# Performance work log

Measured on AMD Instinct MI355X. Metric: run time of the kernel, lower is better.

The kernel has to match this reference:

```python
import jax, jax.numpy as jnp
import numpy as np

HID = 64
PRE = 14


def _lstm_last(x, Wih, Whh, b):
    # x: (B, T, F) batch_first; single-layer torch LSTM; returns last hidden (B, H)
    H = Whh.shape[1]
    def step(carry, xt):
        h, c = carry
        g = xt @ Wih.T + h @ Whh.T + b  # gates order i,f,g,o (torch convention)
        i, f, gg, o = jnp.split(g, 4, axis=-1)
        c = jax.nn.sigmoid(f) * c + jax.nn.sigmoid(i) * jnp.tanh(gg)
        h = jax.nn.sigmoid(o) * jnp.tanh(c)
        return (h, c), None
    h0 = jnp.zeros((x.shape[0], H), x.dtype)
    (h, _), _ = jax.lax.scan(step, (h0, h0), jnp.swapaxes(x, 0, 1))
    return h


def _sircell(beta, gamma, c, sir):
    # beta,gamma: (B,N,1); c: (B,N,N); sir: (B,N,3); beta_incorporated=False branch
    eps = 1e-8
    S, I, R = sir[..., 0:1], sir[..., 1:2], sir[..., 2:3]
    Ntot = jnp.maximum(S + I + R, eps)
    infection = c @ I                      # (B,N,1) graph diffusion of infected
    dS = -beta * S / Ntot * infection
    dI = -dS - gamma * I
    dR = gamma * I
    S_t = jnp.maximum(S + dS, 0.0)
    I_t = jnp.maximum(I + dI, 0.0)
    R_t = jnp.maximum(R + dR, 0.0)
    scale = Ntot / jnp.maximum(S_t + I_t + R_t, eps)
    I_new = jnp.maximum(-dS, 0.0)
    return jnp.concatenate([I_new, S_t * scale, I_t * scale, R_t * scale], axis=-1)


def reference(x_s, x, bWih, bWhh, bb, bfW, bfb, gWih, gWhh, gb, gfW, gfb, cWih, cWhh, cb, cfW, cfb):
    B, T, N, F = x_s.shape
    P = bfW.shape[0]
    xs = jnp.transpose(x_s, (0, 2, 1, 3)).reshape(B * N, T, F)
    betas = jax.nn.sigmoid(_lstm_last(xs, bWih, bWhh, bb) @ bfW.T + bfb).reshape(B, N, P, 1)
    gammas = jax.nn.sigmoid(_lstm_last(xs, gWih, gWhh, gb) @ gfW.T + gfb).reshape(B, N, P, 1)
    xst = jnp.transpose(x_s, (0, 2, 1, 3))                       # (B,N,T,F)
    Hi = jnp.broadcast_to(xst[:, :, None], (B, N, N, T, F))
    Hj = jnp.broadcast_to(xst[:, None], (B, N, N, T, F))
    edge = jnp.concatenate([Hi, Hj], -1).reshape(B * N * N, T, 2 * F)
    cij = jax.nn.sigmoid(_lstm_last(edge, cWih, cWhh, cb) @ cfW.T + cfb).reshape(B, N, N, P)
    cij = jax.nn.softmax(jnp.transpose(cij, (0, 3, 1, 2)), axis=-1)  # (B,P,N,N)
    cs = jnp.transpose(cij, (0, 2, 1, 3))                            # (B,N,P,N)

    def step(sir, inp):
        bt, gt, ct = inp
        nsir = _sircell(bt, gt, ct, sir)
        return nsir[:, :, 1:], nsir

    _, outs = jax.lax.scan(
        step, x[:, -1],
        (jnp.transpose(betas, (2, 0, 1, 3)),
         jnp.transpose(gammas, (2, 0, 1, 3)),
         jnp.transpose(cs, (2, 0, 1, 3))))
    out = jnp.transpose(outs, (1, 0, 2, 3))                          # (B,P,N,4)
    epi = jnp.transpose(jnp.concatenate([betas, gammas, cs], -1), (0, 2, 1, 3))  # (B,P,N,N+2)
    return out[..., 2:3], epi, out[..., 1:], out[..., 0:1]


def setup_inputs() -> dict:
    key = jax.random.key(0)
    ks = jax.random.split(key, 20)
    B, T, N, F = 4, 12, 128, 3
    H, P = HID, PRE
    s = 1.0 / np.sqrt(H)
    def u(k, shape):
        return jax.random.uniform(k, shape, jnp.float32, -s, s)
    inp = {
        'x_s': jax.random.normal(ks[0], (B, T, N, F), jnp.float32),
        'x': jax.random.uniform(ks[1], (B, T, N, F), jnp.float32),
        'bWih': u(ks[2], (4 * H, F)), 'bWhh': u(ks[3], (4 * H, H)), 'bb': u(ks[4], (4 * H,)),
        'bfW': u(ks[5], (P, H)), 'bfb': u(ks[6], (P,)),
        'gWih': u(ks[7], (4 * H, F)), 'gWhh': u(ks[8], (4 * H, H)), 'gb': u(ks[9], (4 * H,)),
        'gfW': u(ks[10], (P, H)), 'gfb': u(ks[11], (P,)),
        'cWih': u(ks[12], (4 * H, 2 * F)), 'cWhh': u(ks[13], (4 * H, H)), 'cb': u(ks[14], (4 * H,)),
        'cfW': u(ks[15], (P, H)), 'cfb': u(ks[16], (P,)),
    }
    return inp
```

## Files before the change

kernel.cpp:

```cpp
#include <hip/hip_runtime.h>

#define TT 12
#define NN 128
#define BB 4
#define PP 14

typedef __attribute__((ext_vector_type(8))) short short8;
typedef __attribute__((ext_vector_type(4))) float f32x4;
typedef __attribute__((ext_vector_type(2))) float float2v;
typedef __attribute__((ext_vector_type(2))) unsigned uint2v;

__device__ inline unsigned short f2bf(float x){
  unsigned u = __builtin_bit_cast(unsigned, x);
  u += 0x7fffu + ((u >> 16) & 1u);
  return (unsigned short)(u >> 16);
}
__device__ inline float bf2f(unsigned short h){
  unsigned u = ((unsigned)h) << 16;
  return __builtin_bit_cast(float, u);
}
__device__ inline float fexp2(float x){ return __builtin_amdgcn_exp2f(x); }
__device__ inline float frcp(float x){ return __builtin_amdgcn_rcpf(x); }
__device__ inline float sigf(float x){ return frcp(1.0f + fexp2(x * -1.44269504f)); }

__device__ inline float2v exp2v(float2v x){
  float2v r; r[0]=__builtin_amdgcn_exp2f(x[0]); r[1]=__builtin_amdgcn_exp2f(x[1]); return r;
}
__device__ inline float2v rcpv1(float2v x){
  float r = frcp(x[0]*x[1]);
  float2v o; o[0] = x[1]*r; o[1] = x[0]*r; return o;
}

__global__ __launch_bounds__(512) void lstm_all(
    const float* __restrict__ x_s,
    const float* __restrict__ bWih, const float* __restrict__ bWhh, const float* __restrict__ bb_,
    const float* __restrict__ bfW,  const float* __restrict__ bfb,
    const float* __restrict__ gWih, const float* __restrict__ gWhh, const float* __restrict__ gb_,
    const float* __restrict__ gfW,  const float* __restrict__ gfb,
    const float* __restrict__ cWih, const float* __restrict__ cWhh, const float* __restrict__ cb_,
    const float* __restrict__ cfW,  const float* __restrict__ cfb,
    float* __restrict__ out_epi)
{
  __shared__ __align__(16) unsigned short wfrag[48*64*8];
  __shared__ __align__(16) char hbuf[2*8192];
  __shared__ __align__(16) unsigned short xext[TT*64*8];
  __shared__ unsigned short fw_lds[PP*64];
  __shared__ float fb_lds[PP];

  const int tid = threadIdx.x;
  const int l = tid & 63;
  const int wv = tid >> 6;
  const int w_h = wv & 3;
  const int half = wv >> 2;
  const int col = l & 15, q = l >> 4;

  const int rot = (col & 7) << 4;
  const int rowA = half*32 + col,  rowB = half*32 + 16 + col;
  const int r0offA = rowA*128 + (((q<<4) + rot) & 127);
  const int r1offA = rowA*128 + ((64 + (q<<4) + rot) & 127);
  const int r0offB = rowB*128 + (((q<<4) + rot) & 127);
  const int r1offB = rowB*128 + ((64 + (q<<4) + rot) & 127);
  const int wroffA = rowA*128 + ((w_h*32 + q*8 + rot) & 127);
  const int wroffB = rowB*128 + ((w_h*32 + q*8 + rot) & 127);

  int g = blockIdx.x;
  int mode; const float *Wih, *Whh, *bias, *fW, *fb;
  if (g < 1024)      { mode=0; Wih=cWih; Whh=cWhh; bias=cb_; fW=cfW; fb=cfb; }
  else if (g < 1032) { mode=1; g-=1024; Wih=bWih; Whh=bWhh; bias=bb_; fW=bfW; fb=bfb; }
  else               { mode=2; g-=1032; Wih=gWih; Whh=gWhh; bias=gb_; fW=gfW; fb=gfb; }

  int b, i=0, s0;
  if (mode==0) { b = g >> 8; int rem = g & 255; i = rem >> 1; s0 = (rem & 1) << 6; }
  else         { b = g >> 1; s0 = (g & 1) << 6; }

  for (int task = tid; task < TT*64; task += 512) {
    int t = task >> 6, m = task & 63;
    unsigned short* dst = &xext[(t*64+m)*8];
    float v0=0,v1=0,v2=0,v3=0,v4=0,v5=0,v6=0,v7=0;
    if (mode==0) {
      const float* xi = x_s + ((b*TT + t)*NN + i)*3;
      const float* xj = x_s + ((b*TT + t)*NN + (s0+m))*3;
      v0=xi[0]; v1=xi[1]; v2=xi[2]; v3=xj[0]; v4=xj[1]; v5=xj[2]; v6=1.f;
    } else {
      const float* xn = x_s + ((b*TT + t)*NN + (s0+m))*3;
      v0=xn[0]; v1=xn[1]; v2=xn[2]; v3=1.f;
    }
    dst[0]=f2bf(v0); dst[1]=f2bf(v1); dst[2]=f2bf(v2); dst[3]=f2bf(v3);
    dst[4]=f2bf(v4); dst[5]=f2bf(v5); dst[6]=f2bf(v6); dst[7]=f2bf(v7);
  }
  for (int idx = tid; idx < 2048; idx += 512) ((unsigned*)hbuf)[idx] = 0;
  for (int idx = tid; idx < PP*64; idx += 512) fw_lds[idx] = f2bf(fW[idx]);
  if (tid < PP) fb_lds[tid] = fb[tid];

  for (int slot = tid; slot < 48*64; slot += 512) {
    int tile = slot >> 6, lane = slot & 63;
    int w_hs = tile / 12, rem = tile % 12, gt = rem / 3, kt = rem % 3;
    float sc = (gt==2) ? 2.88539008f : -1.44269504f;
    int gate = gt*64 + w_hs*16 + (lane & 15);
    int qq = lane >> 4;
    short8 fr = {0,0,0,0,0,0,0,0};
    if (kt < 2) {
      const float* src = Whh + gate*64 + kt*32 + qq*8;
      #pragma unroll
      for (int jj = 0; jj < 8; ++jj) fr[jj] = (short)f2bf(src[jj]*sc);
    } else if (qq == 0) {
      if (mode==0) {
        fr[0]=(short)f2bf(Wih[gate*6+0]*sc); fr[1]=(short)f2bf(Wih[gate*6+1]*sc); fr[2]=(short)f2bf(Wih[gate*6+2]*sc);
        fr[3]=(short)f2bf(Wih[gate*6+3]*sc); fr[4]=(short)f2bf(Wih[gate*6+4]*sc); fr[5]=(short)f2bf(Wih[gate*6+5]*sc);
        fr[6]=(short)f2bf(bias[gate]*sc);
      } else {
        fr[0]=(short)f2bf(Wih[gate*3+0]*sc); fr[1]=(short)f2bf(Wih[gate*3+1]*sc); fr[2]=(short)f2bf(Wih[gate*3+2]*sc);
        fr[3]=(short)f2bf(bias[gate]*sc);
      }
    }
    *(short8*)&wfrag[slot*8] = fr;
  }

  __syncthreads();

  float2v cA0 = {0.f,0.f}, cA1 = {0.f,0.f}, cB0 = {0.f,0.f}, cB1 = {0.f,0.f};

#define MM(acc, aop, bop) acc = __builtin_amdgcn_mfma_f32_16x16x32_bf16(aop, bop, acc, 0,0,0)
#define CELL(cvar, hvar, fF, fI, fG, fO) { \
    float2v Ei = exp2v(fI), Ef = exp2v(fF), Eg = exp2v(fG), Eo = exp2v(fO); \
    float2v t1 = (Ei + 1.0f) * (Eg + 1.0f); \
    float2v pf = Ef + 1.0f; \
    float2v num = cvar * t1 + pf * (Eg - 1.0f); \
    cvar = num * rcpv1(pf * t1); \
    float2v Ec = exp2v(cvar * 2.88539008f); \
    hvar = (Ec - 1.0f) * rcpv1((Ec + 1.0f) * (Eo + 1.0f)); }
#define GATETILE(gt, accA, accB) { \
    short8 f0 = *(const short8*)&wfrag[((w_h*12 + (gt)*3 + 0)*64 + l)*8]; \
    short8 f1 = *(const short8*)&wfrag[((w_h*12 + (gt)*3 + 1)*64 + l)*8]; \
    short8 fx = *(const short8*)&wfrag[((w_h*12 + (gt)*3 + 2)*64 + l)*8]; \
    MM(accA, f0, b0a); MM(accB, f0, b0b); \
    MM(accA, f1, b1a); MM(accB, f1, b1b); \
    MM(accA, fx, bxa); MM(accB, fx, bxb); }

  for (int t = 0; t < TT; ++t) {
    const char* rb = hbuf + ((t & 1) ? 8192 : 0);
    char* wbp      = hbuf + ((t & 1) ? 0 : 8192);
    short8 b0a = *(const short8*)(rb + r0offA);
    short8 b1a = *(const short8*)(rb + r1offA);
    short8 b0b = *(const short8*)(rb + r0offB);
    short8 b1b = *(const short8*)(rb + r1offB);
    short8 bxa = *(const short8*)&xext[(t*64 + half*32 + col)*8];
    short8 bxb = *(const short8*)&xext[(t*64 + half*32 + 16 + col)*8];
    f32x4 Fa = {0.f,0.f,0.f,0.f}, Ia = Fa, Ga = Fa, Oa = Fa;
    f32x4 Fb = Fa, Ib = Fa, Gb = Fa, Ob = Fa;
    GATETILE(1, Fa, Fb);
    GATETILE(0, Ia, Ib);
    GATETILE(2, Ga, Gb);
    GATETILE(3, Oa, Ob);

    {
      float2v f0 = {Fa[0],Fa[1]}, f1 = {Fa[2],Fa[3]};
      float2v i0 = {Ia[0],Ia[1]}, i1 = {Ia[2],Ia[3]};
      float2v g0v = {Ga[0],Ga[1]}, g1v = {Ga[2],Ga[3]};
      float2v o0 = {Oa[0],Oa[1]}, o1 = {Oa[2],Oa[3]};
      float2v h0, h1;
      CELL(cA0, h0, f0, i0, g0v, o0);
      CELL(cA1, h1, f1, i1, g1v, o1);
      unsigned plo, phi;
      asm("v_cvt_pk_bf16_f32 %0, %1, %2" : "=v"(plo) : "v"(h0[0]), "v"(h0[1]));
      asm("v_cvt_pk_bf16_f32 %0, %1, %2" : "=v"(phi) : "v"(h1[0]), "v"(h1[1]));
      uint2v pv = {plo, phi};
      *(uint2v*)(wbp + wroffA) = pv;
    }
    {
      float2v f0 = {Fb[0],Fb[1]}, f1 = {Fb[2],Fb[3]};
      float2v i0 = {Ib[0],Ib[1]}, i1 = {Ib[2],Ib[3]};
      float2v g0v = {Gb[0],Gb[1]}, g1v = {Gb[2],Gb[3]};
      float2v o0 = {Ob[0],Ob[1]}, o1 = {Ob[2],Ob[3]};
      float2v h0, h1;
      CELL(cB0, h0, f0, i0, g0v, o0);
      CELL(cB1, h1, f1, i1, g1v, o1);
      unsigned plo, phi;
      asm("v_cvt_pk_bf16_f32 %0, %1, %2" : "=v"(plo) : "v"(h0[0]), "v"(h0[1]));
      asm("v_cvt_pk_bf16_f32 %0, %1, %2" : "=v"(phi) : "v"(h1[0]), "v"(h1[1]));
      uint2v pv = {plo, phi};
      *(uint2v*)(wbp + wroffB) = pv;
    }
    __syncthreads();
  }
#undef MM
#undef CELL
#undef GATETILE

  const char* hfin = hbuf;
  for (int task = tid; task < 64*PP; task += 512) {
    int seq = task & 63, p = task >> 6;
    int rot2 = (seq & 7) << 4;
    float dot = fb_lds[p];
    #pragma unroll
    for (int kc = 0; kc < 8; ++kc) {
      short8 v = *(const short8*)(hfin + seq*128 + (((kc<<4) + rot2) & 127));
      #pragma unroll
      for (int jj = 0; jj < 8; ++jj)
        dot += bf2f((unsigned short)v[jj]) * bf2f(fw_lds[p*64 + kc*8 + jj]);
    }
    float val = sigf(dot);
    if (mode==0) {
      out_epi[(size_t)((b*PP + p)*NN + i)*130 + 2 + (s0+seq)] = val;
    } else if (mode==1) {
      out_epi[(size_t)((b*PP + p)*NN + (s0+seq))*130 + 0] = val;
    } else {
      out_epi[(size_t)((b*PP + p)*NN + (s0+seq))*130 + 1] = val;
    }
  }
}

__global__ __launch_bounds__(256) void softmax_epi(float* __restrict__ out_epi)
{
  int row = blockIdx.x*4 + (threadIdx.x >> 6);
  int l = threadIdx.x & 63;
  float* epi = out_epi + (size_t)row*130;
  float v0 = epi[2+l], v1 = epi[2+64+l];
  float e0 = fexp2(v0*1.44269504f), e1 = fexp2(v1*1.44269504f);
  float s = e0 + e1;
  #pragma unroll
  for (int off = 32; off; off >>= 1) s += __shfl_xor(s, off);
  float inv = frcp(s);
  epi[2+l] = e0*inv; epi[2+64+l] = e1*inv;
}

__global__ __launch_bounds__(1024) void sir_scan(
    const float* __restrict__ x,
    const float* __restrict__ epi,
    float* __restrict__ out0, float* __restrict__ out2, float* __restrict__ out3)
{
  __shared__ float Ish[NN];
  int b = blockIdx.x;
  int tid = threadIdx.x;
  int i = tid >> 3, q = tid & 7;
  const float* x0 = x + ((b*TT + 11)*NN + i)*3;
  float S = x0[0], I = x0[1], R = x0[2];
  if (q == 0) Ish[i] = I;

  float2v v[8], vn[8];
  {
    const float* crow = epi + (size_t)((b*PP + 0)*NN + i)*130 + 2 + q*16;
    #pragma unroll
    for (int jj = 0; jj < 8; ++jj) v[jj] = *(const float2v*)(crow + jj*2);
  }
  __syncthreads();
  for (int p = 0; p < PP; ++p) {
    if (p+1 < PP) {
      const float* crow = epi + (size_t)((b*PP + p+1)*NN + i)*130 + 2 + q*16;
      #pragma unroll
      for (int jj = 0; jj < 8; ++jj) vn[jj] = *(const float2v*)(crow + jj*2);
    }
    float part = 0.f;
    #pragma unroll
    for (int jj = 0; jj < 8; ++jj)
      part += v[jj][0]*Ish[q*16 + jj*2] + v[jj][1]*Ish[q*16 + jj*2 + 1];
    part += __shfl_xor(part, 1);
    part += __shfl_xor(part, 2);
    part += __shfl_xor(part, 4);
    __syncthreads();
    if (q == 0) {
      const float* erow = epi + (size_t)((b*PP + p)*NN + i)*130;
      float beta  = erow[0];
      float gamma = erow[1];
      float Ntot = fmaxf(S+I+R, 1e-8f);
      float dS = -beta*S/Ntot*part;
      float dI = -dS - gamma*I;
      float dR = gamma*I;
      float St = fmaxf(S+dS, 0.f), It = fmaxf(I+dI, 0.f), Rt = fmaxf(R+dR, 0.f);
      float scale = Ntot / fmaxf(St+It+Rt, 1e-8f);
      float Inew = fmaxf(-dS, 0.f);
      int o = (b*PP+p)*NN + i;
      float Sn = St*scale, In = It*scale, Rn = Rt*scale;
      out0[o] = In;
      out2[o*3+0] = Sn; out2[o*3+1] = In; out2[o*3+2] = Rn;
      out3[o] = Inew;
      S = Sn; I = In; R = Rn;
      Ish[i] = I;
    }
    #pragma unroll
    for (int jj = 0; jj < 8; ++jj) v[jj] = vn[jj];
    __syncthreads();
  }
}

extern "C" void kernel_launch(void* const* d_in, const int* in_sizes, int n_in,
                              void* d_out, int out_size, void* d_ws, size_t ws_size,
                              hipStream_t stream) {
  const float* x_s  = (const float*)d_in[0];
  const float* x    = (const float*)d_in[1];
  const float* bWih = (const float*)d_in[2];
  const float* bWhh = (const float*)d_in[3];
  const float* bb_  = (const float*)d_in[4];
  const float* bfW  = (const float*)d_in[5];
  const float* bfb  = (const float*)d_in[6];
  const float* gWih = (const float*)d_in[7];
  const float* gWhh = (const float*)d_in[8];
  const float* gb_  = (const float*)d_in[9];
  const float* gfW  = (const float*)d_in[10];
  const float* gfb  = (const float*)d_in[11];
  const float* cWih = (const float*)d_in[12];
  const float* cWhh = (const float*)d_in[13];
  const float* cb_  = (const float*)d_in[14];
  const float* cfW  = (const float*)d_in[15];
  const float* cfb  = (const float*)d_in[16];

  float* out  = (float*)d_out;
  float* out0 = out;
  float* epi  = out + 7168;
  float* out2 = out + 7168 + 931840;
  float* out3 = out + 7168 + 931840 + 21504;

  hipLaunchKernelGGL(lstm_all, dim3(1040), dim3(512), 0, stream,
      x_s, bWih,bWhh,bb_,bfW,bfb, gWih,gWhh,gb_,gfW,gfb, cWih,cWhh,cb_,cfW,cfb,
      epi);
  hipLaunchKernelGGL(softmax_epi, dim3(1792), dim3(256), 0, stream, epi);
  hipLaunchKernelGGL(sir_scan, dim3(4), dim3(1024), 0, stream,
      x, epi, out0, out2, out3);
}
```

Before: 107.4 us.

## Give each wave its own sequences so LSTM steps skip block barriers

The LSTM kernel now runs 256 threads per block instead of 512. Each wave owns 16 sequences and computes all four hidden-slice gate tiles for them, keeping its hidden state in a private LDS scratch area. This removes the double-buffered shared hidden state and the __syncthreads at every time step, and the final projection is done per wave. In exchange each wave issues twice as many serial MFMAs per step. Block-level parallelism per CU also drops, because the large LDS weight footprint still limits how many blocks fit per CU.

```diff
diff --git a/kernel.cpp b/kernel.cpp
--- a/kernel.cpp
+++ b/kernel.cpp
@@ -31,7 +31,7 @@
   float2v o; o[0] = x[1]*r; o[1] = x[0]*r; return o;
 }
 
-__global__ __launch_bounds__(512) void lstm_all(
+__global__ __launch_bounds__(256) void lstm_all(
     const float* __restrict__ x_s,
     const float* __restrict__ bWih, const float* __restrict__ bWhh, const float* __restrict__ bb_,
     const float* __restrict__ bfW,  const float* __restrict__ bfb,
@@ -42,7 +42,7 @@
     float* __restrict__ out_epi)
 {
   __shared__ __align__(16) unsigned short wfrag[48*64*8];
-  __shared__ __align__(16) char hbuf[2*8192];
+  __shared__ __align__(16) char hscratch[4*2048];
   __shared__ __align__(16) unsigned short xext[TT*64*8];
   __shared__ unsigned short fw_lds[PP*64];
   __shared__ float fb_lds[PP];
@@ -50,18 +50,12 @@
   const int tid = threadIdx.x;
   const int l = tid & 63;
   const int wv = tid >> 6;
-  const int w_h = wv & 3;
-  const int half = wv >> 2;
   const int col = l & 15, q = l >> 4;
 
   const int rot = (col & 7) << 4;
-  const int rowA = half*32 + col,  rowB = half*32 + 16 + col;
-  const int r0offA = rowA*128 + (((q<<4) + rot) & 127);
-  const int r1offA = rowA*128 + ((64 + (q<<4) + rot) & 127);
-  const int r0offB = rowB*128 + (((q<<4) + rot) & 127);
-  const int r1offB = rowB*128 + ((64 + (q<<4) + rot) & 127);
-  const int wroffA = rowA*128 + ((w_h*32 + q*8 + rot) & 127);
-  const int wroffB = rowB*128 + ((w_h*32 + q*8 + rot) & 127);
+  char* hs = hscratch + wv*2048;
+  const int r0off = col*128 + (((q<<4) + rot) & 127);
+  const int r1off = col*128 + ((64 + (q<<4) + rot) & 127);
 
   int g = blockIdx.x;
   int mode; const float *Wih, *Whh, *bias, *fW, *fb;
@@ -73,7 +67,7 @@
   if (mode==0) { b = g >> 8; int rem = g & 255; i = rem >> 1; s0 = (rem & 1) << 6; }
   else         { b = g >> 1; s0 = (g & 1) << 6; }
 
-  for (int task = tid; task < TT*64; task += 512) {
+  for (int task = tid; task < TT*64; task += 256) {
     int t = task >> 6, m = task & 63;
     unsigned short* dst = &xext[(t*64+m)*8];
     float v0=0,v1=0,v2=0,v3=0,v4=0,v5=0,v6=0,v7=0;
@@ -88,11 +82,11 @@
     dst[0]=f2bf(v0); dst[1]=f2bf(v1); dst[2]=f2bf(v2); dst[3]=f2bf(v3);
     dst[4]=f2bf(v4); dst[5]=f2bf(v5); dst[6]=f2bf(v6); dst[7]=f2bf(v7);
   }
-  for (int idx = tid; idx < 2048; idx += 512) ((unsigned*)hbuf)[idx] = 0;
-  for (int idx = tid; idx < PP*64; idx += 512) fw_lds[idx] = f2bf(fW[idx]);
+  for (int idx = tid; idx < PP*64; idx += 256) fw_lds[idx] = f2bf(fW[idx]);
   if (tid < PP) fb_lds[tid] = fb[tid];
-
-  for (int slot = tid; slot < 48*64; slot += 512) {
+  for (int idx = l; idx < 512; idx += 64) ((unsigned*)hs)[idx] = 0;
+
+  for (int slot = tid; slot < 48*64; slot += 256) {
     int tile = slot >> 6, lane = slot & 63;
     int w_hs = tile / 12, rem = tile % 12, gt = rem / 3, kt = rem % 3;
     float sc = (gt==2) ? 2.88539008f : -1.44269504f;
@@ -118,7 +112,9 @@
 
   __syncthreads();
 
-  float2v cA0 = {0.f,0.f}, cA1 = {0.f,0.f}, cB0 = {0.f,0.f}, cB1 = {0.f,0.f};
+  float2v c0s[4], c1s[4];
+  #pragma unroll
+  for (int s = 0; s < 4; ++s) { c0s[s] = (float2v){0.f,0.f}; c1s[s] = (float2v){0.f,0.f}; }
 
 #define MM(acc, aop, bop) acc = __builtin_amdgcn_mfma_f32_16x16x32_bf16(aop, bop, acc, 0,0,0)
 #define CELL(cvar, hvar, fF, fI, fG, fO) { \
@@ -129,77 +125,57 @@
     cvar = num * rcpv1(pf * t1); \
     float2v Ec = exp2v(cvar * 2.88539008f); \
     hvar = (Ec - 1.0f) * rcpv1((Ec + 1.0f) * (Eo + 1.0f)); }
-#define GATETILE(gt, accA, accB) { \
-    short8 f0 = *(const short8*)&wfrag[((w_h*12 + (gt)*3 + 0)*64 + l)*8]; \
-    short8 f1 = *(const short8*)&wfrag[((w_h*12 + (gt)*3 + 1)*64 + l)*8]; \
-    short8 fx = *(const short8*)&wfrag[((w_h*12 + (gt)*3 + 2)*64 + l)*8]; \
-    MM(accA, f0, b0a); MM(accB, f0, b0b); \
-    MM(accA, f1, b1a); MM(accB, f1, b1b); \
-    MM(accA, fx, bxa); MM(accB, fx, bxb); }
 
   for (int t = 0; t < TT; ++t) {
-    const char* rb = hbuf + ((t & 1) ? 8192 : 0);
-    char* wbp      = hbuf + ((t & 1) ? 0 : 8192);
-    short8 b0a = *(const short8*)(rb + r0offA);
-    short8 b1a = *(const short8*)(rb + r1offA);
-    short8 b0b = *(const short8*)(rb + r0offB);
-    short8 b1b = *(const short8*)(rb + r1offB);
-    short8 bxa = *(const short8*)&xext[(t*64 + half*32 + col)*8];
-    short8 bxb = *(const short8*)&xext[(t*64 + half*32 + 16 + col)*8];
-    f32x4 Fa = {0.f,0.f,0.f,0.f}, Ia = Fa, Ga = Fa, Oa = Fa;
-    f32x4 Fb = Fa, Ib = Fa, Gb = Fa, Ob = Fa;
-    GATETILE(1, Fa, Fb);
-    GATETILE(0, Ia, Ib);
-    GATETILE(2, Ga, Gb);
-    GATETILE(3, Oa, Ob);
-
-    {
-      float2v f0 = {Fa[0],Fa[1]}, f1 = {Fa[2],Fa[3]};
-      float2v i0 = {Ia[0],Ia[1]}, i1 = {Ia[2],Ia[3]};
-      float2v g0v = {Ga[0],Ga[1]}, g1v = {Ga[2],Ga[3]};
-      float2v o0 = {Oa[0],Oa[1]}, o1 = {Oa[2],Oa[3]};
+    short8 b0 = *(const short8*)(hs + r0off);
+    short8 b1 = *(const short8*)(hs + r1off);
+    short8 bx = *(const short8*)&xext[(t*64 + wv*16 + col)*8];
+    #pragma unroll
+    for (int s = 0; s < 4; ++s) {
+      const unsigned short* wb = &wfrag[((s*12)*64 + l)*8];
+      f32x4 Fv = {0.f,0.f,0.f,0.f}, Iv = Fv, Gv = Fv, Ov = Fv;
+      MM(Fv, *(const short8*)(wb + 3*512), b0);
+      MM(Iv, *(const short8*)(wb + 0*512), b0);
+      MM(Gv, *(const short8*)(wb + 6*512), b0);
+      MM(Ov, *(const short8*)(wb + 9*512), b0);
+      MM(Fv, *(const short8*)(wb + 4*512), b1);
+      MM(Iv, *(const short8*)(wb + 1*512), b1);
+      MM(Gv, *(const short8*)(wb + 7*512), b1);
+      MM(Ov, *(const short8*)(wb + 10*512), b1);
+      MM(Fv, *(const short8*)(wb + 5*512), bx);
+      MM(Iv, *(const short8*)(wb + 2*512), bx);
+      MM(Gv, *(const short8*)(wb + 8*512), bx);
+      MM(Ov, *(const short8*)(wb + 11*512), bx);
+      float2v f0 = {Fv[0],Fv[1]}, f1 = {Fv[2],Fv[3]};
+      float2v i0 = {Iv[0],Iv[1]}, i1 = {Iv[2],Iv[3]};
+      float2v g0v = {Gv[0],Gv[1]}, g1v = {Gv[2],Gv[3]};
+      float2v o0 = {Ov[0],Ov[1]}, o1 = {Ov[2],Ov[3]};
       float2v h0, h1;
-      CELL(cA0, h0, f0, i0, g0v, o0);
-      CELL(cA1, h1, f1, i1, g1v, o1);
+      CELL(c0s[s], h0, f0, i0, g0v, o0);
+      CELL(c1s[s], h1, f1, i1, g1v, o1);
       unsigned plo, phi;
       asm("v_cvt_pk_bf16_f32 %0, %1, %2" : "=v"(plo) : "v"(h0[0]), "v"(h0[1]));
       asm("v_cvt_pk_bf16_f32 %0, %1, %2" : "=v"(phi) : "v"(h1[0]), "v"(h1[1]));
       uint2v pv = {plo, phi};
-      *(uint2v*)(wbp + wroffA) = pv;
-    }
-    {
-      float2v f0 = {Fb[0],Fb[1]}, f1 = {Fb[2],Fb[3]};
-      float2v i0 = {Ib[0],Ib[1]}, i1 = {Ib[2],Ib[3]};
-      float2v g0v = {Gb[0],Gb[1]}, g1v = {Gb[2],Gb[3]};
-      float2v o0 = {Ob[0],Ob[1]}, o1 = {Ob[2],Ob[3]};
-      float2v h0, h1;
-      CELL(cB0, h0, f0, i0, g0v, o0);
-      CELL(cB1, h1, f1, i1, g1v, o1);
-      unsigned plo, phi;
-      asm("v_cvt_pk_bf16_f32 %0, %1, %2" : "=v"(plo) : "v"(h0[0]), "v"(h0[1]));
-      asm("v_cvt_pk_bf16_f32 %0, %1, %2" : "=v"(phi) : "v"(h1[0]), "v"(h1[1]));
-      uint2v pv = {plo, phi};
-      *(uint2v*)(wbp + wroffB) = pv;
-    }
-    __syncthreads();
+      *(uint2v*)(hs + col*128 + ((s*32 + q*8 + rot) & 127)) = pv;
+    }
   }
 #undef MM
 #undef CELL
-#undef GATETILE
-
-  const char* hfin = hbuf;
-  for (int task = tid; task < 64*PP; task += 512) {
-    int seq = task & 63, p = task >> 6;
-    int rot2 = (seq & 7) << 4;
+
+  for (int task = l; task < 16*PP; task += 64) {
+    int sl = task & 15, p = task >> 4;
+    int rot2 = (sl & 7) << 4;
     float dot = fb_lds[p];
     #pragma unroll
     for (int kc = 0; kc < 8; ++kc) {
-      short8 v = *(const short8*)(hfin + seq*128 + (((kc<<4) + rot2) & 127));
+      short8 v = *(const short8*)(hs + sl*128 + (((kc<<4) + rot2) & 127));
       #pragma unroll
       for (int jj = 0; jj < 8; ++jj)
         dot += bf2f((unsigned short)v[jj]) * bf2f(fw_lds[p*64 + kc*8 + jj]);
     }
     float val = sigf(dot);
+    int seq = wv*16 + sl;
     if (mode==0) {
       out_epi[(size_t)((b*PP + p)*NN + i)*130 + 2 + (s0+seq)] = val;
     } else if (mode==1) {
@@ -310,7 +286,7 @@
   float* out2 = out + 7168 + 931840;
   float* out3 = out + 7168 + 931840 + 21504;
 
-  hipLaunchKernelGGL(lstm_all, dim3(1040), dim3(512), 0, stream,
+  hipLaunchKernelGGL(lstm_all, dim3(1040), dim3(256), 0, stream,
       x_s, bWih,bWhh,bb_,bfW,bfb, gWih,gWhh,gb_,gfW,gfb, cWih,cWhh,cb_,cfW,cfb,
       epi);
   hipLaunchKernelGGL(softmax_epi, dim3(1792), dim3(256), 0, stream, epi);
```

After: 121.2 us. +12.9%, slower.
